# Performance work log

Measured on AMD Instinct MI355X. Metric: run time of the kernel, lower is better.

The kernel has to match this reference:

```python
import jax, jax.numpy as jnp
import numpy as np

N_NODES = 100000
N_EDGES = 1600000
D_IN = 128
D_OUT = 128
K_HOPS = 2


def gcn_norm(edge_index, num_nodes):
    # Add self-loops (weight 1), compute symmetric normalization
    # norm_e = deg^{-1/2}[src] * deg^{-1/2}[dst], deg over destination index.
    loop = jnp.arange(num_nodes, dtype=edge_index.dtype)
    src = jnp.concatenate([edge_index[0], loop])
    dst = jnp.concatenate([edge_index[1], loop])
    w = jnp.ones(src.shape[0], dtype=jnp.float32)
    deg = jax.ops.segment_sum(w, dst, num_segments=num_nodes)
    dinv = jnp.where(deg > 0, jax.lax.rsqrt(deg), 0.0)
    norm = dinv[src] * dinv[dst]
    return src, dst, norm


def setup_inputs() -> dict:
    key = jax.random.key(0)
    k1, k2, k3, k4 = jax.random.split(key, 4)
    x = jax.random.normal(k1, (N_NODES, D_IN), dtype=jnp.float32)
    edge_index = jax.random.randint(k2, (2, N_EDGES), 0, N_NODES, dtype=jnp.int64)
    # SGConv linear params (Glorot-ish scale)
    W = jax.random.normal(k3, (D_IN, D_OUT), dtype=jnp.float32) / np.sqrt(D_IN)
    b = jnp.zeros((D_OUT,), dtype=jnp.float32)
    return {"x": x, "edge_index": edge_index, "W": W, "b": b}


def reference(x, edge_index, W, b):
    n = x.shape[0]
    src, dst, norm = gcn_norm(edge_index, n)
    h = x
    for _ in range(K_HOPS):
        # gather source features, scale by edge norm, scatter-add to destinations
        h = jax.ops.segment_sum(h[src] * norm[:, None], dst, num_segments=n)
    return h @ W + b
```

## Files before the change

kernel.cpp:

```cpp
#include <hip/hip_runtime.h>
#include <hip/hip_bf16.h>


#define DFEAT 128
#define ELLW 64
#define ABLK 4096
#define CAP 4608
#define NBUCKMAX 512

typedef __attribute__((ext_vector_type(8))) short short8;
typedef __attribute__((ext_vector_type(4))) float f32x4;
typedef __attribute__((ext_vector_type(4))) unsigned int u32x4;
typedef __attribute__((ext_vector_type(4))) int i32x4;

__device__ __forceinline__ float bf2f(unsigned short u) {
    union { unsigned int i; float f; } t;
    t.i = ((unsigned int)u) << 16;
    return t.f;
}

__device__ __forceinline__ unsigned short f2bf(float f) {
    union { float f; unsigned int i; } t;
    t.f = f;
    unsigned int lsb = (t.i >> 16) & 1u;
    t.i += 0x7fffu + lsb;
    return (unsigned short)(t.i >> 16);
}

__device__ __forceinline__ void accum8(float* acc, uint4 u, float w) {
    acc[0] += bf2f((unsigned short)(u.x & 0xffffu)) * w;
    acc[1] += bf2f((unsigned short)(u.x >> 16)) * w;
    acc[2] += bf2f((unsigned short)(u.y & 0xffffu)) * w;
    acc[3] += bf2f((unsigned short)(u.y >> 16)) * w;
    acc[4] += bf2f((unsigned short)(u.z & 0xffffu)) * w;
    acc[5] += bf2f((unsigned short)(u.z >> 16)) * w;
    acc[6] += bf2f((unsigned short)(u.w & 0xffffu)) * w;
    acc[7] += bf2f((unsigned short)(u.w >> 16)) * w;
}

__device__ __forceinline__ void add8(float* acc, uint4 u) {
    union { unsigned int i; float f; } a;
    a.i = u.x << 16;          acc[0] += a.f;
    a.i = u.x & 0xffff0000u;  acc[1] += a.f;
    a.i = u.y << 16;          acc[2] += a.f;
    a.i = u.y & 0xffff0000u;  acc[3] += a.f;
    a.i = u.z << 16;          acc[4] += a.f;
    a.i = u.z & 0xffff0000u;  acc[5] += a.f;
    a.i = u.w << 16;          acc[6] += a.f;
    a.i = u.w & 0xffff0000u;  acc[7] += a.f;
}

__global__ void k_detect(const unsigned short* __restrict__ xs,
                         const int* __restrict__ ei, int* __restrict__ flags) {
    int t = blockIdx.x * 256 + (int)threadIdx.x;
    int bad = 0;
    for (int i = t; i < 16384; i += 2048) {
        unsigned int e = (xs[i] >> 7) & 0xFFu;
        if (e >= 0xC0u) bad = 1;
    }
    if (__any(bad) && (threadIdx.x & 63) == 0) atomicOr(flags, 1);
    int oddnz = 0;
    for (int i = t; i < 4096; i += 2048) {
        if (ei[2 * i + 1] != 0) oddnz = 1;
    }
    if (__any(oddnz) && (threadIdx.x & 63) == 0) atomicOr(flags + 1, 1);
}

__global__ void k_prepB(const void* __restrict__ Wraw, const int* __restrict__ flags,
                        unsigned short* __restrict__ Bf) {
    int t = blockIdx.x * 256 + threadIdx.x;
    if (t >= 2048) return;
    int lane = t & 63;
    int chunk = (t >> 6) & 3;
    int ntile = t >> 8;
    int ncol = ntile * 16 + (lane & 15);
    int k0 = chunk * 32 + (lane >> 4) * 8;
    int isf = flags[0];
    const float* Wf = (const float*)Wraw;
    const unsigned short* Wb = (const unsigned short*)Wraw;
    unsigned short* o = Bf + (size_t)t * 8;
#pragma unroll
    for (int j = 0; j < 8; j++) {
        int idx = (k0 + j) * DFEAT + ncol;
        o[j] = isf ? f2bf(Wf[idx]) : Wb[idx];
    }
}

__global__ __launch_bounds__(256) void k_bucketA(const int* __restrict__ ei, int E, int n,
                                                 const int* __restrict__ flags,
                                                 int* __restrict__ bucketCnt,
                                                 unsigned int* __restrict__ buck) {
    __shared__ int sd[ABLK];
    __shared__ int hist[NBUCKMAX];
    __shared__ int base_[NBUCKMAX];
    for (int t = threadIdx.x; t < NBUCKMAX; t += 256) hist[t] = 0;
    __syncthreads();
    int e0 = blockIdx.x * ABLK;
    int e1 = min(E, e0 + ABLK);
    int i64 = (flags[1] == 0);
    for (int e = e0 + (int)threadIdx.x; e < e1; e += 256) {
        int d = i64 ? __builtin_nontemporal_load(ei + 2 * (E + e))
                    : __builtin_nontemporal_load(ei + E + e);
        sd[e - e0] = d;
        atomicAdd(&hist[d >> 8], 1);
    }
    __syncthreads();
#pragma unroll
    for (int r = 0; r < 2; r++) {
        int t = ((int)threadIdx.x + r * 256 + (int)blockIdx.x * 61) & (NBUCKMAX - 1);
        int cc = hist[t];
        base_[t] = cc ? atomicAdd(bucketCnt + t, cc) : 0;
        hist[t] = 0;
    }
    __syncthreads();
    for (int e = e0 + (int)threadIdx.x; e < e1; e += 256) {
        int d = sd[e - e0];
        int s = i64 ? __builtin_nontemporal_load(ei + 2 * e)
                    : __builtin_nontemporal_load(ei + e);
        int b = d >> 8;
        int pos = base_[b] + atomicAdd(&hist[b], 1);
        if (pos < CAP)
            buck[(size_t)b * CAP + pos] = (unsigned int)s | ((unsigned int)(d & 255) << 17);
    }
}

__global__ __launch_bounds__(256) void k_bucketB(const unsigned int* __restrict__ buck,
                                                 const int* __restrict__ bucketCnt, int n,
                                                 int* __restrict__ cnt,
                                                 int* __restrict__ ell) {
    __shared__ int lcnt[256];
    int b = blockIdx.x;
    lcnt[threadIdx.x] = 0;
    __syncthreads();
    int m = min(bucketCnt[b], CAP);
    int node0 = b << 8;
    const unsigned int* bp = buck + (size_t)b * CAP;
    for (int i = threadIdx.x; i < m; i += 256) {
        unsigned int w = __builtin_nontemporal_load(bp + i);
        int s = (int)(w & 0x1FFFFu);
        int dl = (int)(w >> 17);
        int pos = atomicAdd(&lcnt[dl], 1);
        if (pos < ELLW) ell[(size_t)(node0 + dl) * ELLW + pos] = s;
    }
    __syncthreads();
    int node = node0 + (int)threadIdx.x;
    if (node < n) {
        int c = lcnt[threadIdx.x];
        cnt[node] = c;
        int st = min(c, ELLW);
        int slots = min((c + 16) & ~15, ELLW);
        int* rowp = ell + (size_t)node * ELLW;
        for (int p = st; p < slots; p++) rowp[p] = node;
    }
}

__global__ __launch_bounds__(256) void k_gemm0(const void* __restrict__ xraw,
                                               const unsigned short* __restrict__ Bf,
                                               const int* __restrict__ flags,
                                               const int* __restrict__ cnt,
                                               unsigned short* __restrict__ g0, int n) {
    __shared__ unsigned short thi[16 * 136];
    __shared__ unsigned short tlo[16 * 136];
    int wave = threadIdx.x >> 6;
    int lane = threadIdx.x & 63;
    int g = lane >> 4, c = lane & 15;
    int trow = wave * 4 + g;
    int node = blockIdx.x * 16 + trow;
    int isf = flags[0];

    uint4 ohi = {0, 0, 0, 0}, olo = {0, 0, 0, 0};
    if (node < n) {
        if (isf) {
            const float* xf = (const float*)xraw;
            f32x4 v0 = __builtin_nontemporal_load((const f32x4*)(xf + (size_t)node * DFEAT + c * 8));
            f32x4 v1 = __builtin_nontemporal_load((const f32x4*)(xf + (size_t)node * DFEAT + c * 8 + 4));
            float vv[8] = {v0[0], v0[1], v0[2], v0[3], v1[0], v1[1], v1[2], v1[3]};
            unsigned short h[8], l[8];
#pragma unroll
            for (int j = 0; j < 8; j++) {
                h[j] = f2bf(vv[j]);
                l[j] = f2bf(vv[j] - bf2f(h[j]));
            }
            ohi.x = (unsigned int)h[0] | ((unsigned int)h[1] << 16);
            ohi.y = (unsigned int)h[2] | ((unsigned int)h[3] << 16);
            ohi.z = (unsigned int)h[4] | ((unsigned int)h[5] << 16);
            ohi.w = (unsigned int)h[6] | ((unsigned int)h[7] << 16);
            olo.x = (unsigned int)l[0] | ((unsigned int)l[1] << 16);
            olo.y = (unsigned int)l[2] | ((unsigned int)l[3] << 16);
            olo.z = (unsigned int)l[4] | ((unsigned int)l[5] << 16);
            olo.w = (unsigned int)l[6] | ((unsigned int)l[7] << 16);
        } else {
            u32x4 u = __builtin_nontemporal_load(
                (const u32x4*)((const unsigned short*)xraw + (size_t)node * DFEAT + c * 8));
            ohi.x = u[0]; ohi.y = u[1]; ohi.z = u[2]; ohi.w = u[3];
        }
    }
    *(uint4*)(thi + trow * 136 + c * 8) = ohi;
    *(uint4*)(tlo + trow * 136 + c * 8) = olo;
    __syncthreads();

    int m = c, quad = g;
    f32x4 acc2[2];
    acc2[0] = (f32x4){0.f, 0.f, 0.f, 0.f};
    acc2[1] = (f32x4){0.f, 0.f, 0.f, 0.f};
#pragma unroll
    for (int c2 = 0; c2 < 4; c2++) {
        short8 ah = *(const short8*)(thi + m * 136 + c2 * 32 + quad * 8);
        short8 al = *(const short8*)(tlo + m * 136 + c2 * 32 + quad * 8);
#pragma unroll
        for (int t = 0; t < 2; t++) {
            int nt = wave * 2 + t;
            short8 bfr = *(const short8*)(Bf + ((size_t)(nt * 4 + c2) * 64 + lane) * 8);
            acc2[t] = __builtin_amdgcn_mfma_f32_16x16x32_bf16(ah, bfr, acc2[t], 0, 0, 0);
            acc2[t] = __builtin_amdgcn_mfma_f32_16x16x32_bf16(al, bfr, acc2[t], 0, 0, 0);
        }
    }

    float sc[4];
#pragma unroll
    for (int r2 = 0; r2 < 4; r2++) {
        int grow = blockIdx.x * 16 + quad * 4 + r2;
        sc[r2] = (grow < n) ? rsqrtf((float)(cnt[grow] + 1)) : 0.f;
    }
#pragma unroll
    for (int t = 0; t < 2; t++) {
        int col = (wave * 2 + t) * 16 + m;
#pragma unroll
        for (int r2 = 0; r2 < 4; r2++) {
            int grow = blockIdx.x * 16 + quad * 4 + r2;
            if (grow < n)
                __builtin_nontemporal_store(f2bf(acc2[t][r2] * sc[r2]),
                                            g0 + (size_t)grow * DFEAT + col);
        }
    }
}

__device__ __forceinline__ void hop_accum(const unsigned short* __restrict__ fb,
                                          const int* __restrict__ ell,
                                          int node, int cn, int lane, float* acc) {
    int g = lane >> 4, c = lane & 15;
    int slots = min((cn + 16) & ~15, ELLW);
    const int* row = ell + (size_t)node * ELLW;
#pragma unroll
    for (int j = 0; j < 8; j++) acc[j] = 0.f;

    for (int base = 0; base < slots; base += 16) {
        i32x4 s4 = __builtin_nontemporal_load((const i32x4*)(row + base) + g);
        uint4 u0 = *(const uint4*)(fb + (size_t)s4[0] * DFEAT + c * 8);
        uint4 u1 = *(const uint4*)(fb + (size_t)s4[1] * DFEAT + c * 8);
        uint4 u2 = *(const uint4*)(fb + (size_t)s4[2] * DFEAT + c * 8);
        uint4 u3 = *(const uint4*)(fb + (size_t)s4[3] * DFEAT + c * 8);
        add8(acc, u0);
        add8(acc, u1);
        add8(acc, u2);
        add8(acc, u3);
    }
    float corrw = (cn < ELLW) ? (float)(cn + 1 - slots) : 1.0f;
    if (g == 0 && corrw != 0.0f) {
        uint4 u = *(const uint4*)(fb + (size_t)node * DFEAT + c * 8);
        accum8(acc, u, corrw);
    }
#pragma unroll
    for (int j = 0; j < 8; j++) {
        acc[j] += __shfl_xor(acc[j], 16);
        acc[j] += __shfl_xor(acc[j], 32);
    }
}

__global__ __launch_bounds__(256) void k_hop(const unsigned short* __restrict__ src,
                                             const int* __restrict__ ell,
                                             const int* __restrict__ cnt,
                                             unsigned short* __restrict__ outb, int n) {
    int node = blockIdx.x * 4 + (threadIdx.x >> 6);
    if (node >= n) return;
    int lane = threadIdx.x & 63;
    int cn = cnt[node];
    float acc[8];
    hop_accum(src, ell, node, cn, lane, acc);
    if ((lane >> 4) == 0) {
        int c = lane & 15;
        float sc = 1.0f / (float)(cn + 1);
        uint4 o;
        o.x = (unsigned int)f2bf(acc[0] * sc) | ((unsigned int)f2bf(acc[1] * sc) << 16);
        o.y = (unsigned int)f2bf(acc[2] * sc) | ((unsigned int)f2bf(acc[3] * sc) << 16);
        o.z = (unsigned int)f2bf(acc[4] * sc) | ((unsigned int)f2bf(acc[5] * sc) << 16);
        o.w = (unsigned int)f2bf(acc[6] * sc) | ((unsigned int)f2bf(acc[7] * sc) << 16);
        *(uint4*)(outb + (size_t)node * DFEAT + c * 8) = o;
    }
}

__global__ __launch_bounds__(256) void k_hop2_out(const unsigned short* __restrict__ src,
                                                  const int* __restrict__ ell,
                                                  const int* __restrict__ cnt,
                                                  const void* __restrict__ braw,
                                                  const int* __restrict__ flags,
                                                  void* __restrict__ outraw, int n) {
    int node = blockIdx.x * 4 + (threadIdx.x >> 6);
    if (node >= n) return;
    int lane = threadIdx.x & 63;
    int cn = cnt[node];
    float acc[8];
    hop_accum(src, ell, node, cn, lane, acc);
    if ((lane >> 4) == 0) {
        int c = lane & 15;
        float sc = rsqrtf((float)(cn + 1));
        int isf = flags[0];
        const float* bf32 = (const float*)braw;
        const unsigned short* bb16 = (const unsigned short*)braw;
#pragma unroll
        for (int j = 0; j < 8; j++) {
            float bias = isf ? bf32[c * 8 + j] : bf2f(bb16[c * 8 + j]);
            acc[j] = acc[j] * sc + bias;
        }
        if (isf) {
            float* outf = (float*)outraw;
            *(float4*)(outf + (size_t)node * DFEAT + c * 8) =
                (float4){acc[0], acc[1], acc[2], acc[3]};
            *(float4*)(outf + (size_t)node * DFEAT + c * 8 + 4) =
                (float4){acc[4], acc[5], acc[6], acc[7]};
        } else {
            unsigned short* outb = (unsigned short*)outraw;
            uint4 o;
            o.x = (unsigned int)f2bf(acc[0]) | ((unsigned int)f2bf(acc[1]) << 16);
            o.y = (unsigned int)f2bf(acc[2]) | ((unsigned int)f2bf(acc[3]) << 16);
            o.z = (unsigned int)f2bf(acc[4]) | ((unsigned int)f2bf(acc[5]) << 16);
            o.w = (unsigned int)f2bf(acc[6]) | ((unsigned int)f2bf(acc[7]) << 16);
            *(uint4*)(outb + (size_t)node * DFEAT + c * 8) = o;
        }
    }
}

extern "C" void kernel_launch(void* const* d_in, const int* in_sizes, int n_in,
                              void* d_out, int out_size, void* d_ws, size_t ws_size,
                              hipStream_t stream) {
    const void* x = d_in[0];
    const int* ei = (const int*)d_in[1];
    const void* W = d_in[2];
    const void* b = d_in[3];

    const int n = in_sizes[0] / DFEAT;
    const int E = in_sizes[1] / 2;

    int* ell = (int*)d_ws;
    unsigned short* g1 = (unsigned short*)(ell + (size_t)n * ELLW);
    int* cnt = (int*)(g1 + (size_t)n * DFEAT);
    int* flags = cnt + n;
    int* bucketCnt = flags + 4;
    unsigned short* Bf = (unsigned short*)(bucketCnt + NBUCKMAX);
    unsigned short* g0 = (unsigned short*)d_out;
    unsigned int* buck = (unsigned int*)((char*)d_out + (size_t)out_size
                                         - (size_t)NBUCKMAX * CAP * 4);

    (void)hipMemsetAsync(flags, 0, (4 + NBUCKMAX) * sizeof(int), stream);

    k_detect<<<8, 256, 0, stream>>>((const unsigned short*)x, ei, flags);

    k_prepB<<<8, 256, 0, stream>>>(W, flags, Bf);

    int nbuck = (n + 255) >> 8;
    int ablocks = (E + ABLK - 1) / ABLK;
    k_bucketA<<<ablocks, 256, 0, stream>>>(ei, E, n, flags, bucketCnt, buck);
    k_bucketB<<<nbuck, 256, 0, stream>>>(buck, bucketCnt, n, cnt, ell);

    k_gemm0<<<(n + 15) / 16, 256, 0, stream>>>(x, Bf, flags, cnt, g0, n);

    k_hop<<<(n + 3) / 4, 256, 0, stream>>>(g0, ell, cnt, g1, n);

    k_hop2_out<<<(n + 3) / 4, 256, 0, stream>>>(g1, ell, cnt, b, flags, d_out, n);
}
```

Baseline: 316.4 us.

## Fuse ELL bucket finalization with initial X·W GEMM per 256-node block

Merges the bucketB ELL-building kernel and the gemm0 kernel so that each 256-node bucket block also computes the bf16 X·W product for its 256 nodes in 16 tiles, reading degrees from shared memory instead of global cnt. The bucket scratch is moved from the tail of the output buffer to the g1 workspace, since the fused kernel now writes g0 into the output while the bucket data is still being read. This saves a launch and a global cnt round trip, but gemm parallelism drops from about 6250 blocks to about 391, with serialized tiles and extra barriers per block. Stores to g0 switch from nontemporal to regular.

```diff
diff --git a/kernel.cpp b/kernel.cpp
--- a/kernel.cpp
+++ b/kernel.cpp
@@ -124,18 +124,25 @@
     }
 }
 
-__global__ __launch_bounds__(256) void k_bucketB(const unsigned int* __restrict__ buck,
-                                                 const int* __restrict__ bucketCnt, int n,
-                                                 int* __restrict__ cnt,
-                                                 int* __restrict__ ell) {
+__global__ __launch_bounds__(256) void k_bucketB_gemm0(
+        const unsigned int* __restrict__ buck,
+        const int* __restrict__ bucketCnt, int n,
+        int* __restrict__ cnt, int* __restrict__ ell,
+        const void* __restrict__ xraw,
+        const unsigned short* __restrict__ Bf,
+        const int* __restrict__ flags,
+        unsigned short* __restrict__ g0) {
     __shared__ int lcnt[256];
+    __shared__ unsigned short thi[16 * 136];
+    __shared__ unsigned short tlo[16 * 136];
     int b = blockIdx.x;
     lcnt[threadIdx.x] = 0;
     __syncthreads();
-    int m = min(bucketCnt[b], CAP);
+
+    int m0 = min(bucketCnt[b], CAP);
     int node0 = b << 8;
     const unsigned int* bp = buck + (size_t)b * CAP;
-    for (int i = threadIdx.x; i < m; i += 256) {
+    for (int i = threadIdx.x; i < m0; i += 256) {
         unsigned int w = __builtin_nontemporal_load(bp + i);
         int s = (int)(w & 0x1FFFFu);
         int dl = (int)(w >> 17);
@@ -143,94 +150,91 @@
         if (pos < ELLW) ell[(size_t)(node0 + dl) * ELLW + pos] = s;
     }
     __syncthreads();
-    int node = node0 + (int)threadIdx.x;
-    if (node < n) {
-        int c = lcnt[threadIdx.x];
-        cnt[node] = c;
-        int st = min(c, ELLW);
-        int slots = min((c + 16) & ~15, ELLW);
-        int* rowp = ell + (size_t)node * ELLW;
-        for (int p = st; p < slots; p++) rowp[p] = node;
-    }
-}
-
-__global__ __launch_bounds__(256) void k_gemm0(const void* __restrict__ xraw,
-                                               const unsigned short* __restrict__ Bf,
-                                               const int* __restrict__ flags,
-                                               const int* __restrict__ cnt,
-                                               unsigned short* __restrict__ g0, int n) {
-    __shared__ unsigned short thi[16 * 136];
-    __shared__ unsigned short tlo[16 * 136];
+    {
+        int node = node0 + (int)threadIdx.x;
+        if (node < n) {
+            int c = lcnt[threadIdx.x];
+            cnt[node] = c;
+            int st = min(c, ELLW);
+            int slots = min((c + 16) & ~15, ELLW);
+            int* rowp = ell + (size_t)node * ELLW;
+            for (int p = st; p < slots; p++) rowp[p] = node;
+        }
+    }
+
+    int isf = flags[0];
     int wave = threadIdx.x >> 6;
     int lane = threadIdx.x & 63;
     int g = lane >> 4, c = lane & 15;
     int trow = wave * 4 + g;
-    int node = blockIdx.x * 16 + trow;
-    int isf = flags[0];
-
-    uint4 ohi = {0, 0, 0, 0}, olo = {0, 0, 0, 0};
-    if (node < n) {
-        if (isf) {
-            const float* xf = (const float*)xraw;
-            f32x4 v0 = __builtin_nontemporal_load((const f32x4*)(xf + (size_t)node * DFEAT + c * 8));
-            f32x4 v1 = __builtin_nontemporal_load((const f32x4*)(xf + (size_t)node * DFEAT + c * 8 + 4));
-            float vv[8] = {v0[0], v0[1], v0[2], v0[3], v1[0], v1[1], v1[2], v1[3]};
-            unsigned short h[8], l[8];
-#pragma unroll
-            for (int j = 0; j < 8; j++) {
-                h[j] = f2bf(vv[j]);
-                l[j] = f2bf(vv[j] - bf2f(h[j]));
+
+    for (int tile = 0; tile < 16; ++tile) {
+        int lrow = tile * 16 + trow;
+        int node = node0 + lrow;
+        uint4 ohi = {0, 0, 0, 0}, olo = {0, 0, 0, 0};
+        if (node < n) {
+            if (isf) {
+                const float* xf = (const float*)xraw;
+                f32x4 v0 = __builtin_nontemporal_load((const f32x4*)(xf + (size_t)node * DFEAT + c * 8));
+                f32x4 v1 = __builtin_nontemporal_load((const f32x4*)(xf + (size_t)node * DFEAT + c * 8 + 4));
+                float vv[8] = {v0[0], v0[1], v0[2], v0[3], v1[0], v1[1], v1[2], v1[3]};
+                unsigned short h[8], l[8];
+#pragma unroll
+                for (int j = 0; j < 8; j++) {
+                    h[j] = f2bf(vv[j]);
+                    l[j] = f2bf(vv[j] - bf2f(h[j]));
+                }
+                ohi.x = (unsigned int)h[0] | ((unsigned int)h[1] << 16);
+                ohi.y = (unsigned int)h[2] | ((unsigned int)h[3] << 16);
+                ohi.z = (unsigned int)h[4] | ((unsigned int)h[5] << 16);
+                ohi.w = (unsigned int)h[6] | ((unsigned int)h[7] << 16);
+                olo.x = (unsigned int)l[0] | ((unsigned int)l[1] << 16);
+                olo.y = (unsigned int)l[2] | ((unsigned int)l[3] << 16);
+                olo.z = (unsigned int)l[4] | ((unsigned int)l[5] << 16);
+                olo.w = (unsigned int)l[6] | ((unsigned int)l[7] << 16);
+            } else {
+                u32x4 u = __builtin_nontemporal_load(
+                    (const u32x4*)((const unsigned short*)xraw + (size_t)node * DFEAT + c * 8));
+                ohi.x = u[0]; ohi.y = u[1]; ohi.z = u[2]; ohi.w = u[3];
             }
-            ohi.x = (unsigned int)h[0] | ((unsigned int)h[1] << 16);
-            ohi.y = (unsigned int)h[2] | ((unsigned int)h[3] << 16);
-            ohi.z = (unsigned int)h[4] | ((unsigned int)h[5] << 16);
-            ohi.w = (unsigned int)h[6] | ((unsigned int)h[7] << 16);
-            olo.x = (unsigned int)l[0] | ((unsigned int)l[1] << 16);
-            olo.y = (unsigned int)l[2] | ((unsigned int)l[3] << 16);
-            olo.z = (unsigned int)l[4] | ((unsigned int)l[5] << 16);
-            olo.w = (unsigned int)l[6] | ((unsigned int)l[7] << 16);
-        } else {
-            u32x4 u = __builtin_nontemporal_load(
-                (const u32x4*)((const unsigned short*)xraw + (size_t)node * DFEAT + c * 8));
-            ohi.x = u[0]; ohi.y = u[1]; ohi.z = u[2]; ohi.w = u[3];
-        }
-    }
-    *(uint4*)(thi + trow * 136 + c * 8) = ohi;
-    *(uint4*)(tlo + trow * 136 + c * 8) = olo;
-    __syncthreads();
-
-    int m = c, quad = g;
-    f32x4 acc2[2];
-    acc2[0] = (f32x4){0.f, 0.f, 0.f, 0.f};
-    acc2[1] = (f32x4){0.f, 0.f, 0.f, 0.f};
-#pragma unroll
-    for (int c2 = 0; c2 < 4; c2++) {
-        short8 ah = *(const short8*)(thi + m * 136 + c2 * 32 + quad * 8);
-        short8 al = *(const short8*)(tlo + m * 136 + c2 * 32 + quad * 8);
+        }
+        __syncthreads();
+        *(uint4*)(thi + trow * 136 + c * 8) = ohi;
+        *(uint4*)(tlo + trow * 136 + c * 8) = olo;
+        __syncthreads();
+
+        int m = c, quad = g;
+        f32x4 acc2[2];
+        acc2[0] = (f32x4){0.f, 0.f, 0.f, 0.f};
+        acc2[1] = (f32x4){0.f, 0.f, 0.f, 0.f};
+#pragma unroll
+        for (int c2 = 0; c2 < 4; c2++) {
+            short8 ah = *(const short8*)(thi + m * 136 + c2 * 32 + quad * 8);
+            short8 al = *(const short8*)(tlo + m * 136 + c2 * 32 + quad * 8);
+#pragma unroll
+            for (int t = 0; t < 2; t++) {
+                int nt = wave * 2 + t;
+                short8 bfr = *(const short8*)(Bf + ((size_t)(nt * 4 + c2) * 64 + lane) * 8);
+                acc2[t] = __builtin_amdgcn_mfma_f32_16x16x32_bf16(ah, bfr, acc2[t], 0, 0, 0);
+                acc2[t] = __builtin_amdgcn_mfma_f32_16x16x32_bf16(al, bfr, acc2[t], 0, 0, 0);
+            }
+        }
+
+        float sc[4];
+#pragma unroll
+        for (int r2 = 0; r2 < 4; r2++) {
+            int lr = tile * 16 + quad * 4 + r2;
+            sc[r2] = (node0 + lr < n) ? rsqrtf((float)(lcnt[lr] + 1)) : 0.f;
+        }
 #pragma unroll
         for (int t = 0; t < 2; t++) {
-            int nt = wave * 2 + t;
-            short8 bfr = *(const short8*)(Bf + ((size_t)(nt * 4 + c2) * 64 + lane) * 8);
-            acc2[t] = __builtin_amdgcn_mfma_f32_16x16x32_bf16(ah, bfr, acc2[t], 0, 0, 0);
-            acc2[t] = __builtin_amdgcn_mfma_f32_16x16x32_bf16(al, bfr, acc2[t], 0, 0, 0);
-        }
-    }
-
-    float sc[4];
-#pragma unroll
-    for (int r2 = 0; r2 < 4; r2++) {
-        int grow = blockIdx.x * 16 + quad * 4 + r2;
-        sc[r2] = (grow < n) ? rsqrtf((float)(cnt[grow] + 1)) : 0.f;
-    }
-#pragma unroll
-    for (int t = 0; t < 2; t++) {
-        int col = (wave * 2 + t) * 16 + m;
-#pragma unroll
-        for (int r2 = 0; r2 < 4; r2++) {
-            int grow = blockIdx.x * 16 + quad * 4 + r2;
-            if (grow < n)
-                __builtin_nontemporal_store(f2bf(acc2[t][r2] * sc[r2]),
-                                            g0 + (size_t)grow * DFEAT + col);
+            int col = (wave * 2 + t) * 16 + m;
+#pragma unroll
+            for (int r2 = 0; r2 < 4; r2++) {
+                int gnode = node0 + tile * 16 + quad * 4 + r2;
+                if (gnode < n)
+                    g0[(size_t)gnode * DFEAT + col] = f2bf(acc2[t][r2] * sc[r2]);
+            }
         }
     }
 }
@@ -348,8 +352,7 @@
     int* bucketCnt = flags + 4;
     unsigned short* Bf = (unsigned short*)(bucketCnt + NBUCKMAX);
     unsigned short* g0 = (unsigned short*)d_out;
-    unsigned int* buck = (unsigned int*)((char*)d_out + (size_t)out_size
-                                         - (size_t)NBUCKMAX * CAP * 4);
+    unsigned int* buck = (unsigned int*)g1;
 
     (void)hipMemsetAsync(flags, 0, (4 + NBUCKMAX) * sizeof(int), stream);
 
@@ -360,9 +363,9 @@
     int nbuck = (n + 255) >> 8;
     int ablocks = (E + ABLK - 1) / ABLK;
     k_bucketA<<<ablocks, 256, 0, stream>>>(ei, E, n, flags, bucketCnt, buck);
-    k_bucketB<<<nbuck, 256, 0, stream>>>(buck, bucketCnt, n, cnt, ell);
-
-    k_gemm0<<<(n + 15) / 16, 256, 0, stream>>>(x, Bf, flags, cnt, g0, n);
+
+    k_bucketB_gemm0<<<nbuck, 256, 0, stream>>>(buck, bucketCnt, n, cnt, ell,
+                                               x, Bf, flags, g0);
 
     k_hop<<<(n + 3) / 4, 256, 0, stream>>>(g0, ell, cnt, g1, n);
 
```

Result: no change. 313.8 us (-0.8%).
